# Optimization experiments

Measured on AMD Instinct MI355X. Metric: run time of the kernel, lower is better.

The kernel has to match this reference:

```python
import jax, jax.numpy as jnp
import numpy as np
from functools import partial

SEQ, BATCH, HIDDEN = 2048, 4, 2048
FFN = 1408            # swiglu: h_to_4h outputs 2*FFN
N_EXPERTS = 8
TOP_K = 2
EPS = 1e-20


def setup_inputs() -> dict:
    key = jax.random.key(0)
    k0, k1, k2, k3 = jax.random.split(key, 4)
    x = jax.random.normal(k0, (SEQ, BATCH, HIDDEN), dtype=jnp.float32)
    wg = jax.random.normal(k1, (N_EXPERTS, HIDDEN), dtype=jnp.float32) * 0.02
    w1 = jax.random.normal(k2, (N_EXPERTS, HIDDEN, 2 * FFN), dtype=jnp.float32) * 0.02
    w2 = jax.random.normal(k3, (N_EXPERTS, FFN, HIDDEN), dtype=jnp.float32) * 0.02
    return {"x": x, "wg": wg, "w1": w1, "w2": w2}


def reference(x, wg, w1, w2):
    # x: [S, B, H] (Megatron layout); transpose(0,1) as in MoELayer.forward
    S, B, H = x.shape
    T = B * S
    xt = jnp.transpose(x, (1, 0, 2)).reshape(T, H)  # [T, H]

    # --- TopKGate (greedy, softmax scoring, norm_topk_prob=True) ---
    logits = xt @ wg.T                       # [T, E]
    scores = jax.nn.softmax(logits, axis=-1)
    topk_w, topk_i = jax.lax.top_k(scores, TOP_K)          # [T, K]
    topk_w = topk_w / (jnp.sum(topk_w, axis=-1, keepdims=True) + EPS)

    # combine weights per (token, expert): C[t, e] = sum_k w_k * [idx_k == e]
    C = jnp.zeros((T, N_EXPERTS), dtype=xt.dtype)
    C = C.at[jnp.arange(T)[:, None], topk_i].add(topk_w)   # [T, E]

    # --- Experts: per-expert swiglu MLP, accumulate weighted combine ---
    def step(acc, inputs):
        w1e, w2e, ce = inputs                # [H,2F], [F,H], [T]
        h = xt @ w1e                         # [T, 2F]
        a, b = jnp.split(h, 2, axis=-1)
        y = (jax.nn.silu(a) * b) @ w2e       # [T, H]
        return acc + ce[:, None] * y, None

    out0 = jnp.zeros((T, H), dtype=xt.dtype)
    out, _ = jax.lax.scan(step, out0, (w1, w2, C.T))

    # back to [S, B, H]
    return jnp.transpose(out.reshape(B, S, H), (1, 0, 2))
```

## Files before the change

### kernel.cpp

```cpp
#include <hip/hip_runtime.h>
#include <hip/hip_bf16.h>
#include <cstdint>
#include <cstddef>


#define S_ 2048
#define B_ 4
#define H_ 2048
#define F_ 1408
#define F2_ 2816
#define E_ 8
#define T_ 8192

typedef float f32x4 __attribute__((ext_vector_type(4)));
typedef short s16x8 __attribute__((ext_vector_type(8)));

__device__ __forceinline__ unsigned short f2b(float f) {
  union { unsigned int i; float f; } v; v.f = f;
  unsigned int r = v.i + 0x7FFFu + ((v.i >> 16) & 1u);
  return (unsigned short)(r >> 16);
}
__device__ __forceinline__ unsigned int pkbf(float lo, float hi) {
  __hip_bfloat162 h2 = __float22bfloat162_rn(make_float2(lo, hi));
  union { __hip_bfloat162 v; unsigned int u; } c; c.v = h2; return c.u;
}
__device__ __forceinline__ void gld16(const unsigned short* gp, unsigned short* lp) {
  __builtin_amdgcn_global_load_lds(
      (const __attribute__((address_space(1))) unsigned int*)gp,
      (__attribute__((address_space(3))) unsigned int*)lp, 16, 0, 0);
}


__global__ void zero_kernel(int* ws_i) {
  if (threadIdx.x < 16) ws_i[threadIdx.x] = 0;
}

__global__ __launch_bounds__(256) void cvt_kernel(
    const float* __restrict__ src, unsigned short* __restrict__ dst, int n8) {
  int i = blockIdx.x * 256 + threadIdx.x;
  if (i >= n8) return;
  f32x4 a = *(const f32x4*)(src + (size_t)i * 8);
  f32x4 b = *(const f32x4*)(src + (size_t)i * 8 + 4);
  uint4 u;
  u.x = pkbf(a[0], a[1]); u.y = pkbf(a[2], a[3]);
  u.z = pkbf(b[0], b[1]); u.w = pkbf(b[2], b[3]);
  *(uint4*)(dst + (size_t)i * 8) = u;
}

__global__ __launch_bounds__(256) void tcvt_kernel(
    const float* __restrict__ src, unsigned short* __restrict__ dst,
    int rows, int cols) {
  int e = blockIdx.z;
  int c0 = blockIdx.x * 64, r0 = blockIdx.y * 64;
  const float* s = src + (size_t)e * rows * cols;
  unsigned short* d = dst + (size_t)e * rows * cols;
  __shared__ unsigned short Lt[64][72];
  int tid = threadIdx.x;
  int cl = tid & 63, w = tid >> 6;
#pragma unroll
  for (int i = 0; i < 16; i++) {
    int r = w * 16 + i;
    Lt[cl][r] = f2b(s[(size_t)(r0 + r) * cols + c0 + cl]);
  }
  __syncthreads();
  int cc = tid >> 3, hc = tid & 7;
#pragma unroll
  for (int j = 0; j < 2; j++) {
    int c = cc + j * 32;
    *(uint4*)&d[(size_t)(c0 + c) * rows + r0 + hc * 8] = *(uint4*)&Lt[c][hc * 8];
  }
}

__global__ __launch_bounds__(256) void gate_kernel(
    const float* __restrict__ x, const float* __restrict__ wg,
    int* __restrict__ counts, int* __restrict__ eidx, float* __restrict__ ewt) {
  int wave = threadIdx.x >> 6, lane = threadIdx.x & 63;
  int t = blockIdx.x * 4 + wave;
  int b = t >> 11, s = t & (S_ - 1);
  const float* xrow = x + (size_t)(s * B_ + b) * H_;
  float acc[E_];
#pragma unroll
  for (int e = 0; e < E_; e++) acc[e] = 0.f;
  for (int h0 = lane * 4; h0 < H_; h0 += 256) {
    f32x4 xa = *(const f32x4*)(xrow + h0);
#pragma unroll
    for (int e = 0; e < E_; e++) {
      f32x4 wa = *(const f32x4*)(wg + e * H_ + h0);
      acc[e] += xa[0] * wa[0] + xa[1] * wa[1] + xa[2] * wa[2] + xa[3] * wa[3];
    }
  }
#pragma unroll
  for (int e = 0; e < E_; e++)
    for (int off = 32; off; off >>= 1) acc[e] += __shfl_xor(acc[e], off, 64);
  if (lane == 0) {
    float m = acc[0];
#pragma unroll
    for (int e = 1; e < E_; e++) m = fmaxf(m, acc[e]);
    float ex[E_], ssum = 0.f;
#pragma unroll
    for (int e = 0; e < E_; e++) { ex[e] = __expf(acc[e] - m); ssum += ex[e]; }
    float sc[E_];
#pragma unroll
    for (int e = 0; e < E_; e++) sc[e] = ex[e] / ssum;
    int i1 = 0;
#pragma unroll
    for (int e = 1; e < E_; e++) if (sc[e] > sc[i1]) i1 = e;
    int i2 = (i1 == 0) ? 1 : 0;
#pragma unroll
    for (int e = 0; e < E_; e++) if (e != i1 && sc[e] > sc[i2]) i2 = e;
    float wsum = sc[i1] + sc[i2] + 1e-20f;
    eidx[2 * t] = i1;     ewt[2 * t] = sc[i1] / wsum;
    eidx[2 * t + 1] = i2; ewt[2 * t + 1] = sc[i2] / wsum;
    atomicAdd(&counts[i1], 1);
    atomicAdd(&counts[i2], 1);
  }
}

__global__ void scan_kernel(const int* __restrict__ counts, int* __restrict__ offs) {
  if (threadIdx.x == 0) {
    int run = 0;
    for (int e = 0; e < E_; e++) { offs[e] = run; run += counts[e]; }
  }
}

__global__ void assign_kernel(const int* __restrict__ eidx, const float* __restrict__ ewt,
                              const int* __restrict__ offs, int* __restrict__ cursor,
                              int* __restrict__ rowlist, float* __restrict__ rowwt) {
  int t = blockIdx.x * 256 + threadIdx.x;
  if (t >= T_) return;
#pragma unroll
  for (int k = 0; k < 2; k++) {
    int e = eidx[2 * t + k];
    int pos = atomicAdd(&cursor[e], 1);
    int slot = offs[e] + pos;
    rowlist[slot] = t;
    rowwt[slot] = ewt[2 * t + k];
  }
}

__global__ __launch_bounds__(256) void gemm1_kernel(
    const unsigned short* __restrict__ xb, const unsigned short* __restrict__ w1t,
    const int* __restrict__ counts, const int* __restrict__ offs,
    const int* __restrict__ rowlist, unsigned short* __restrict__ g) {
  int e = blockIdx.z, ft = blockIdx.y, rt = blockIdx.x;
  int ne = counts[e];
  if (rt * 128 >= ne) return;
  int base = offs[e];

  __shared__ unsigned short aL[128 * 32];
  __shared__ unsigned short bLa[64 * 32];
  __shared__ unsigned short bLb[64 * 32];

  int tid = threadIdx.x;
  int lane = tid & 63, wave = tid >> 6;
  int wm = (wave & 1) * 64, wn = (wave >> 1) * 32;
  int quad = lane >> 4, l15 = lane & 15;

  int srow = tid >> 2, kc = tid & 3;
  int t0 = rowlist[base + min(rt * 128 + srow, ne - 1)];
  int t1 = rowlist[base + min(rt * 128 + 64 + srow, ne - 1)];
  const unsigned short* ap0 = xb + (size_t)((t0 & (S_ - 1)) * B_ + (t0 >> 11)) * H_ + kc * 8;
  const unsigned short* ap1 = xb + (size_t)((t1 & (S_ - 1)) * B_ + (t1 >> 11)) * H_ + kc * 8;
  const unsigned short* bpa = w1t + ((size_t)e * F2_ + ft * 64 + srow) * H_ + kc * 8;
  const unsigned short* bpb = bpa + (size_t)F_ * H_;

  unsigned short* aD0 = aL + wave * 512;
  unsigned short* aD1 = aL + 2048 + wave * 512;
  unsigned short* bDa = bLa + wave * 512;
  unsigned short* bDb = bLb + wave * 512;

  f32x4 acc[2][4][2];
#pragma unroll
  for (int h2 = 0; h2 < 2; h2++)
    for (int i = 0; i < 4; i++)
      for (int j = 0; j < 2; j++) acc[h2][i][j] = (f32x4){0.f, 0.f, 0.f, 0.f};

  for (int k0 = 0; k0 < H_; k0 += 32) {
    __syncthreads();
    gld16(ap0 + k0, aD0);
    gld16(ap1 + k0, aD1);
    gld16(bpa + k0, bDa);
    gld16(bpb + k0, bDb);
    __syncthreads();

    s16x8 af[4];
#pragma unroll
    for (int mi = 0; mi < 4; mi++)
      af[mi] = *(const s16x8*)&aL[(wm + mi * 16 + l15) * 32 + quad * 8];
    s16x8 bfa[2], bfb[2];
#pragma unroll
    for (int ni = 0; ni < 2; ni++) {
      bfa[ni] = *(const s16x8*)&bLa[(wn + ni * 16 + l15) * 32 + quad * 8];
      bfb[ni] = *(const s16x8*)&bLb[(wn + ni * 16 + l15) * 32 + quad * 8];
    }
#pragma unroll
    for (int mi = 0; mi < 4; mi++)
#pragma unroll
      for (int ni = 0; ni < 2; ni++) {
        acc[0][mi][ni] = __builtin_amdgcn_mfma_f32_16x16x32_bf16(af[mi], bfa[ni], acc[0][mi][ni], 0, 0, 0);
        acc[1][mi][ni] = __builtin_amdgcn_mfma_f32_16x16x32_bf16(af[mi], bfb[ni], acc[1][mi][ni], 0, 0, 0);
      }
  }

#pragma unroll
  for (int mi = 0; mi < 4; mi++)
#pragma unroll
    for (int ni = 0; ni < 2; ni++)
#pragma unroll
      for (int v = 0; v < 4; v++) {
        int row = wm + mi * 16 + quad * 4 + v;
        if (rt * 128 + row < ne) {
          int col = wn + ni * 16 + l15;
          float a = acc[0][mi][ni][v], bb = acc[1][mi][ni][v];
          float sg = a / (1.f + __expf(-a));
          g[(size_t)(base + rt * 128 + row) * F_ + ft * 64 + col] = f2b(sg * bb);
        }
      }
}

__global__ __launch_bounds__(256) void gemm2_kernel(
    const unsigned short* __restrict__ g, const unsigned short* __restrict__ w2t,
    const int* __restrict__ counts, const int* __restrict__ offs,
    const int* __restrict__ rowlist, const float* __restrict__ rowwt,
    float* __restrict__ out) {
  int e = blockIdx.z, nt = blockIdx.y, rt = blockIdx.x;
  int ne = counts[e];
  if (rt * 128 >= ne) return;
  int base = offs[e];

  __shared__ unsigned short aL[128 * 32];
  __shared__ unsigned short bL[128 * 32];
  __shared__ float rwL[128];
  __shared__ int   toL[128];

  int tid = threadIdx.x;
  int lane = tid & 63, wave = tid >> 6;
  int wm = (wave & 1) * 64, wn = (wave >> 1) * 64;
  int quad = lane >> 4, l15 = lane & 15;

  int srow = tid >> 2, kc = tid & 3;
  int r0c = min(rt * 128 + srow, ne - 1);
  int r1c = min(rt * 128 + 64 + srow, ne - 1);
  const unsigned short* ap0 = g + (size_t)(base + r0c) * F_ + kc * 8;
  const unsigned short* ap1 = g + (size_t)(base + r1c) * F_ + kc * 8;
  const unsigned short* bp0 = w2t + ((size_t)e * H_ + nt * 128 + srow) * F_ + kc * 8;
  const unsigned short* bp1 = bp0 + (size_t)64 * F_;

  unsigned short* aD0 = aL + wave * 512;
  unsigned short* aD1 = aL + 2048 + wave * 512;
  unsigned short* bD0 = bL + wave * 512;
  unsigned short* bD1 = bL + 2048 + wave * 512;

  if (tid < 128) {
    int rr = min(rt * 128 + tid, ne - 1);
    rwL[tid] = rowwt[base + rr];
    int tk = rowlist[base + rr];
    toL[tid] = ((tk & (S_ - 1)) * B_ + (tk >> 11)) * H_;
  }

  f32x4 acc[4][4];
#pragma unroll
  for (int i = 0; i < 4; i++)
    for (int j = 0; j < 4; j++) acc[i][j] = (f32x4){0.f, 0.f, 0.f, 0.f};

  for (int k0 = 0; k0 < F_; k0 += 32) {
    __syncthreads();
    gld16(ap0 + k0, aD0);
    gld16(ap1 + k0, aD1);
    gld16(bp0 + k0, bD0);
    gld16(bp1 + k0, bD1);
    __syncthreads();

    s16x8 af[4];
#pragma unroll
    for (int mi = 0; mi < 4; mi++)
      af[mi] = *(const s16x8*)&aL[(wm + mi * 16 + l15) * 32 + quad * 8];
    s16x8 bf[4];
#pragma unroll
    for (int ni = 0; ni < 4; ni++)
      bf[ni] = *(const s16x8*)&bL[(wn + ni * 16 + l15) * 32 + quad * 8];
#pragma unroll
    for (int mi = 0; mi < 4; mi++)
#pragma unroll
      for (int ni = 0; ni < 4; ni++)
        acc[mi][ni] = __builtin_amdgcn_mfma_f32_16x16x32_bf16(af[mi], bf[ni], acc[mi][ni], 0, 0, 0);
  }

#pragma unroll
  for (int mi = 0; mi < 4; mi++)
#pragma unroll
    for (int ni = 0; ni < 4; ni++)
#pragma unroll
      for (int v = 0; v < 4; v++) {
        int row = wm + mi * 16 + quad * 4 + v;
        if (rt * 128 + row < ne) {
          int col = wn + ni * 16 + l15;
          atomicAdd(&out[(size_t)toL[row] + nt * 128 + col], acc[mi][ni][v] * rwL[row]);
        }
      }
}

extern "C" void kernel_launch(void* const* d_in, const int* in_sizes, int n_in,
                              void* d_out, int out_size, void* d_ws, size_t ws_size,
                              hipStream_t stream) {
  const float* x  = (const float*)d_in[0];
  const float* wg = (const float*)d_in[1];
  const float* w1 = (const float*)d_in[2];
  const float* w2 = (const float*)d_in[3];
  float* out = (float*)d_out;

  char* ws = (char*)d_ws;
  int*   counts  = (int*)(ws + 0);
  int*   cursor  = (int*)(ws + 32);
  int*   offs    = (int*)(ws + 64);
  int*   eidx    = (int*)(ws + 128);
  float* ewt     = (float*)(ws + 65664);
  int*   rowlist = (int*)(ws + 131200);
  float* rowwt   = (float*)(ws + 196736);
  unsigned short* g   = (unsigned short*)(ws + 262272);
  unsigned short* xb  = (unsigned short*)(ws + 46399616);
  unsigned short* w1t = (unsigned short*)(ws + 79954048);
  unsigned short* w2t = (unsigned short*)(ws + 172228736);

  hipMemsetAsync(d_out, 0, (size_t)out_size * sizeof(float), stream);
  zero_kernel<<<1, 64, 0, stream>>>((int*)ws);
  cvt_kernel<<<T_ * H_ / 8 / 256, 256, 0, stream>>>(x, xb, T_ * H_ / 8);
  tcvt_kernel<<<dim3(F2_ / 64, H_ / 64, E_), 256, 0, stream>>>(w1, w1t, H_, F2_);
  tcvt_kernel<<<dim3(H_ / 64, F_ / 64, E_), 256, 0, stream>>>(w2, w2t, F_, H_);
  gate_kernel<<<T_ / 4, 256, 0, stream>>>(x, wg, counts, eidx, ewt);
  scan_kernel<<<1, 64, 0, stream>>>(counts, offs);
  assign_kernel<<<T_ / 256, 256, 0, stream>>>(eidx, ewt, offs, cursor, rowlist, rowwt);
  gemm1_kernel<<<dim3(64, 22, E_), 256, 0, stream>>>(xb, w1t, counts, offs, rowlist, g);
  gemm2_kernel<<<dim3(64, 16, E_), 256, 0, stream>>>(g, w2t, counts, offs, rowlist, rowwt, out);
}
```

Baseline: 1.430 ms.

## Double-buffer LDS tiles in both expert GEMMs with manual vmcnt waits

Both grouped GEMM kernels get two LDS buffers per operand. The global-to-LDS loads for the next-but-one K tile are issued right after the current tile's fragments are read into registers, and explicit s_waitcnt/s_barrier calls replace the two __syncthreads per iteration. This is meant to hide global load latency behind the MFMA work. It doubles LDS use per block, which may lower occupancy, and the correctness of the hand-written vmcnt counts depends on each thread issuing exactly four loads per stage.

```diff
diff --git a/kernel.cpp b/kernel.cpp
--- a/kernel.cpp
+++ b/kernel.cpp
@@ -14,6 +14,12 @@
 
 typedef float f32x4 __attribute__((ext_vector_type(4)));
 typedef short s16x8 __attribute__((ext_vector_type(8)));
+
+#define WAITV4 asm volatile("s_waitcnt vmcnt(4)" ::: "memory")
+#define WAITV0 asm volatile("s_waitcnt vmcnt(0)" ::: "memory")
+#define LGKM0  asm volatile("s_waitcnt lgkmcnt(0)" ::: "memory")
+#define SB()   __builtin_amdgcn_s_barrier()
+#define SCB()  __builtin_amdgcn_sched_barrier(0)
 
 __device__ __forceinline__ unsigned short f2b(float f) {
   union { unsigned int i; float f; } v; v.f = f;
@@ -147,9 +153,9 @@
   if (rt * 128 >= ne) return;
   int base = offs[e];
 
-  __shared__ unsigned short aL[128 * 32];
-  __shared__ unsigned short bLa[64 * 32];
-  __shared__ unsigned short bLb[64 * 32];
+  __shared__ unsigned short aL[2][128 * 32];
+  __shared__ unsigned short bLa[2][64 * 32];
+  __shared__ unsigned short bLb[2][64 * 32];
 
   int tid = threadIdx.x;
   int lane = tid & 63, wave = tid >> 6;
@@ -164,43 +170,51 @@
   const unsigned short* bpa = w1t + ((size_t)e * F2_ + ft * 64 + srow) * H_ + kc * 8;
   const unsigned short* bpb = bpa + (size_t)F_ * H_;
 
-  unsigned short* aD0 = aL + wave * 512;
-  unsigned short* aD1 = aL + 2048 + wave * 512;
-  unsigned short* bDa = bLa + wave * 512;
-  unsigned short* bDb = bLb + wave * 512;
-
   f32x4 acc[2][4][2];
 #pragma unroll
   for (int h2 = 0; h2 < 2; h2++)
     for (int i = 0; i < 4; i++)
       for (int j = 0; j < 2; j++) acc[h2][i][j] = (f32x4){0.f, 0.f, 0.f, 0.f};
 
-  for (int k0 = 0; k0 < H_; k0 += 32) {
-    __syncthreads();
-    gld16(ap0 + k0, aD0);
-    gld16(ap1 + k0, aD1);
-    gld16(bpa + k0, bDa);
-    gld16(bpb + k0, bDb);
-    __syncthreads();
-
-    s16x8 af[4];
-#pragma unroll
-    for (int mi = 0; mi < 4; mi++)
-      af[mi] = *(const s16x8*)&aL[(wm + mi * 16 + l15) * 32 + quad * 8];
-    s16x8 bfa[2], bfb[2];
-#pragma unroll
-    for (int ni = 0; ni < 2; ni++) {
-      bfa[ni] = *(const s16x8*)&bLa[(wn + ni * 16 + l15) * 32 + quad * 8];
-      bfb[ni] = *(const s16x8*)&bLb[(wn + ni * 16 + l15) * 32 + quad * 8];
-    }
-#pragma unroll
-    for (int mi = 0; mi < 4; mi++)
-#pragma unroll
-      for (int ni = 0; ni < 2; ni++) {
-        acc[0][mi][ni] = __builtin_amdgcn_mfma_f32_16x16x32_bf16(af[mi], bfa[ni], acc[0][mi][ni], 0, 0, 0);
-        acc[1][mi][ni] = __builtin_amdgcn_mfma_f32_16x16x32_bf16(af[mi], bfb[ni], acc[1][mi][ni], 0, 0, 0);
-      }
-  }
+#define G1STAGE(buf, kk) do {                                  \
+    gld16(ap0 + (kk), &aL[buf][wave * 512]);                   \
+    gld16(ap1 + (kk), &aL[buf][2048 + wave * 512]);            \
+    gld16(bpa + (kk), &bLa[buf][wave * 512]);                  \
+    gld16(bpb + (kk), &bLb[buf][wave * 512]); } while (0)
+
+#define G1COMP(buf) do {                                                         \
+    s16x8 af[4], vfa[2], vfb[2];                                                 \
+    _Pragma("unroll")                                                            \
+    for (int mi = 0; mi < 4; mi++)                                               \
+      af[mi] = *(const s16x8*)&aL[buf][(wm + mi * 16 + l15) * 32 + quad * 8];    \
+    _Pragma("unroll")                                                            \
+    for (int ni = 0; ni < 2; ni++) {                                             \
+      vfa[ni] = *(const s16x8*)&bLa[buf][(wn + ni * 16 + l15) * 32 + quad * 8];  \
+      vfb[ni] = *(const s16x8*)&bLb[buf][(wn + ni * 16 + l15) * 32 + quad * 8];  \
+    }                                                                            \
+    LGKM0; SB(); SCB();                                                          \
+    if (!lastp) { G1STAGE(buf, knext); }                                         \
+    _Pragma("unroll")                                                            \
+    for (int mi = 0; mi < 4; mi++)                                               \
+      _Pragma("unroll")                                                          \
+      for (int ni = 0; ni < 2; ni++) {                                           \
+        acc[0][mi][ni] = __builtin_amdgcn_mfma_f32_16x16x32_bf16(af[mi], vfa[ni], acc[0][mi][ni], 0, 0, 0); \
+        acc[1][mi][ni] = __builtin_amdgcn_mfma_f32_16x16x32_bf16(af[mi], vfb[ni], acc[1][mi][ni], 0, 0, 0); \
+      } } while (0)
+
+  G1STAGE(0, 0);
+  G1STAGE(1, 32);
+
+  for (int k0 = 0; k0 < H_; k0 += 64) {
+    int lastp = (k0 + 64 >= H_);
+    WAITV4; SB(); SCB();
+    { int knext = k0 + 64; G1COMP(0); }
+    if (lastp) { WAITV0; } else { WAITV4; }
+    SB(); SCB();
+    { int knext = k0 + 96; G1COMP(1); }
+  }
+#undef G1STAGE
+#undef G1COMP
 
 #pragma unroll
   for (int mi = 0; mi < 4; mi++)
@@ -228,8 +242,8 @@
   if (rt * 128 >= ne) return;
   int base = offs[e];
 
-  __shared__ unsigned short aL[128 * 32];
-  __shared__ unsigned short bL[128 * 32];
+  __shared__ unsigned short aL[2][128 * 32];
+  __shared__ unsigned short bL[2][128 * 32];
   __shared__ float rwL[128];
   __shared__ int   toL[128];
 
@@ -246,11 +260,6 @@
   const unsigned short* bp0 = w2t + ((size_t)e * H_ + nt * 128 + srow) * F_ + kc * 8;
   const unsigned short* bp1 = bp0 + (size_t)64 * F_;
 
-  unsigned short* aD0 = aL + wave * 512;
-  unsigned short* aD1 = aL + 2048 + wave * 512;
-  unsigned short* bD0 = bL + wave * 512;
-  unsigned short* bD1 = bL + 2048 + wave * 512;
-
   if (tid < 128) {
     int rr = min(rt * 128 + tid, ne - 1);
     rwL[tid] = rowwt[base + rr];
@@ -263,28 +272,42 @@
   for (int i = 0; i < 4; i++)
     for (int j = 0; j < 4; j++) acc[i][j] = (f32x4){0.f, 0.f, 0.f, 0.f};
 
-  for (int k0 = 0; k0 < F_; k0 += 32) {
-    __syncthreads();
-    gld16(ap0 + k0, aD0);
-    gld16(ap1 + k0, aD1);
-    gld16(bp0 + k0, bD0);
-    gld16(bp1 + k0, bD1);
-    __syncthreads();
-
-    s16x8 af[4];
-#pragma unroll
-    for (int mi = 0; mi < 4; mi++)
-      af[mi] = *(const s16x8*)&aL[(wm + mi * 16 + l15) * 32 + quad * 8];
-    s16x8 bf[4];
-#pragma unroll
-    for (int ni = 0; ni < 4; ni++)
-      bf[ni] = *(const s16x8*)&bL[(wn + ni * 16 + l15) * 32 + quad * 8];
-#pragma unroll
-    for (int mi = 0; mi < 4; mi++)
-#pragma unroll
-      for (int ni = 0; ni < 4; ni++)
-        acc[mi][ni] = __builtin_amdgcn_mfma_f32_16x16x32_bf16(af[mi], bf[ni], acc[mi][ni], 0, 0, 0);
-  }
+#define G2STAGE(buf, kk) do {                                  \
+    gld16(ap0 + (kk), &aL[buf][wave * 512]);                   \
+    gld16(ap1 + (kk), &aL[buf][2048 + wave * 512]);            \
+    gld16(bp0 + (kk), &bL[buf][wave * 512]);                   \
+    gld16(bp1 + (kk), &bL[buf][2048 + wave * 512]); } while (0)
+
+#define G2COMP(buf) do {                                                        \
+    s16x8 af[4], bf[4];                                                         \
+    _Pragma("unroll")                                                           \
+    for (int mi = 0; mi < 4; mi++)                                              \
+      af[mi] = *(const s16x8*)&aL[buf][(wm + mi * 16 + l15) * 32 + quad * 8];   \
+    _Pragma("unroll")                                                           \
+    for (int ni = 0; ni < 4; ni++)                                              \
+      bf[ni] = *(const s16x8*)&bL[buf][(wn + ni * 16 + l15) * 32 + quad * 8];   \
+    LGKM0; SB(); SCB();                                                         \
+    if (!lastp) { G2STAGE(buf, knext); }                                        \
+    _Pragma("unroll")                                                           \
+    for (int mi = 0; mi < 4; mi++)                                              \
+      _Pragma("unroll")                                                         \
+      for (int ni = 0; ni < 4; ni++)                                            \
+        acc[mi][ni] = __builtin_amdgcn_mfma_f32_16x16x32_bf16(af[mi], bf[ni], acc[mi][ni], 0, 0, 0); \
+    } while (0)
+
+  G2STAGE(0, 0);
+  G2STAGE(1, 32);
+
+  for (int k0 = 0; k0 < F_; k0 += 64) {
+    int lastp = (k0 + 64 >= F_);
+    WAITV4; SB(); SCB();
+    { int knext = k0 + 64; G2COMP(0); }
+    if (lastp) { WAITV0; } else { WAITV4; }
+    SB(); SCB();
+    { int knext = k0 + 96; G2COMP(1); }
+  }
+#undef G2STAGE
+#undef G2COMP
 
 #pragma unroll
   for (int mi = 0; mi < 4; mi++)
```

New measurement: 1.377 ms. -3.7%, faster.

## Enlarge expert GEMM tiles and double-buffer swizzled LDS loads

Applied to the files above, without the earlier changes.

Both expert GEMMs move from 128-row tiles with a K step of 32 and 256 threads to 256x256 tiles with a K step of 64 and 512 threads. Global-to-LDS loads are double-buffered and issued two stages ahead, gated by explicit vmcnt waits and barriers. An XOR swizzle on the LDS layout avoids bank conflicts, and s_setprio wraps the MFMA bursts. The aim is more data reuse per byte loaded and overlap of memory traffic with matrix math. The cost is 128KB of LDS per block and heavy register use, which limits occupancy, plus more wasted work on partially filled row tiles when an expert has few tokens.

```diff
diff --git a/kernel.cpp b/kernel.cpp
--- a/kernel.cpp
+++ b/kernel.cpp
@@ -15,6 +15,12 @@
 typedef float f32x4 __attribute__((ext_vector_type(4)));
 typedef short s16x8 __attribute__((ext_vector_type(8)));
 
+#define WAITV8 asm volatile("s_waitcnt vmcnt(8)" ::: "memory")
+#define WAITV0 asm volatile("s_waitcnt vmcnt(0)" ::: "memory")
+#define LGKM0  asm volatile("s_waitcnt lgkmcnt(0)" ::: "memory")
+#define SB()   __builtin_amdgcn_s_barrier()
+#define SCB()  __builtin_amdgcn_sched_barrier(0)
+
 __device__ __forceinline__ unsigned short f2b(float f) {
   union { unsigned int i; float f; } v; v.f = f;
   unsigned int r = v.i + 0x7FFFu + ((v.i >> 16) & 1u);
@@ -28,6 +34,9 @@
   __builtin_amdgcn_global_load_lds(
       (const __attribute__((address_space(1))) unsigned int*)gp,
       (__attribute__((address_space(3))) unsigned int*)lp, 16, 0, 0);
+}
+__device__ __forceinline__ s16x8 ldfrag(const unsigned short* base, int r, int c) {
+  return *(const s16x8*)((const char*)base + r * 128 + (((c) ^ (r & 7)) << 4));
 }
 
 
@@ -138,164 +147,270 @@
   }
 }
 
-__global__ __launch_bounds__(256) void gemm1_kernel(
+__global__ __launch_bounds__(512, 2) void gemm1_kernel(
     const unsigned short* __restrict__ xb, const unsigned short* __restrict__ w1t,
     const int* __restrict__ counts, const int* __restrict__ offs,
     const int* __restrict__ rowlist, unsigned short* __restrict__ g) {
-  int e = blockIdx.z, ft = blockIdx.y, rt = blockIdx.x;
+  int e = blockIdx.z, ft = blockIdx.y, mt = blockIdx.x;
   int ne = counts[e];
-  if (rt * 128 >= ne) return;
+  if (mt * 256 >= ne) return;
   int base = offs[e];
 
-  __shared__ unsigned short aL[128 * 32];
-  __shared__ unsigned short bLa[64 * 32];
-  __shared__ unsigned short bLb[64 * 32];
+  __shared__ unsigned short A_[2][256 * 64];
+  __shared__ unsigned short Bt_[2][256 * 64];
 
   int tid = threadIdx.x;
-  int lane = tid & 63, wave = tid >> 6;
-  int wm = (wave & 1) * 64, wn = (wave >> 1) * 32;
-  int quad = lane >> 4, l15 = lane & 15;
-
-  int srow = tid >> 2, kc = tid & 3;
-  int t0 = rowlist[base + min(rt * 128 + srow, ne - 1)];
-  int t1 = rowlist[base + min(rt * 128 + 64 + srow, ne - 1)];
-  const unsigned short* ap0 = xb + (size_t)((t0 & (S_ - 1)) * B_ + (t0 >> 11)) * H_ + kc * 8;
-  const unsigned short* ap1 = xb + (size_t)((t1 & (S_ - 1)) * B_ + (t1 >> 11)) * H_ + kc * 8;
-  const unsigned short* bpa = w1t + ((size_t)e * F2_ + ft * 64 + srow) * H_ + kc * 8;
-  const unsigned short* bpb = bpa + (size_t)F_ * H_;
-
-  unsigned short* aD0 = aL + wave * 512;
-  unsigned short* aD1 = aL + 2048 + wave * 512;
-  unsigned short* bDa = bLa + wave * 512;
-  unsigned short* bDb = bLb + wave * 512;
-
-  f32x4 acc[2][4][2];
-#pragma unroll
-  for (int h2 = 0; h2 < 2; h2++)
-    for (int i = 0; i < 4; i++)
-      for (int j = 0; j < 2; j++) acc[h2][i][j] = (f32x4){0.f, 0.f, 0.f, 0.f};
-
-  for (int k0 = 0; k0 < H_; k0 += 32) {
-    __syncthreads();
-    gld16(ap0 + k0, aD0);
-    gld16(ap1 + k0, aD1);
-    gld16(bpa + k0, bDa);
-    gld16(bpb + k0, bDb);
-    __syncthreads();
-
-    s16x8 af[4];
-#pragma unroll
-    for (int mi = 0; mi < 4; mi++)
-      af[mi] = *(const s16x8*)&aL[(wm + mi * 16 + l15) * 32 + quad * 8];
-    s16x8 bfa[2], bfb[2];
-#pragma unroll
-    for (int ni = 0; ni < 2; ni++) {
-      bfa[ni] = *(const s16x8*)&bLa[(wn + ni * 16 + l15) * 32 + quad * 8];
-      bfb[ni] = *(const s16x8*)&bLb[(wn + ni * 16 + l15) * 32 + quad * 8];
+  int l = tid & 63, w = tid >> 6;
+  int quad = l >> 4, l15 = l & 15;
+  int wmr = (w & 1) * 128;
+  int wn1 = (w >> 1) * 32;
+
+  int r8 = l >> 3, cg = (l & 7) ^ r8;
+  const unsigned short* apt[4];
+  const unsigned short* bpt[4];
+#pragma unroll
+  for (int j = 0; j < 4; j++) {
+    int R = j * 64 + w * 8 + r8;
+    int tok = rowlist[base + min(mt * 256 + R, ne - 1)];
+    apt[j] = xb + (size_t)((tok & (S_ - 1)) * B_ + (tok >> 11)) * H_ + cg * 8;
+    int brow = (R < 128) ? (ft * 128 + R) : (F_ + ft * 128 + (R - 128));
+    bpt[j] = w1t + ((size_t)e * F2_ + brow) * H_ + cg * 8;
+  }
+
+  f32x4 aa[8][2], ab[8][2];
+#pragma unroll
+  for (int i = 0; i < 8; i++)
+#pragma unroll
+    for (int n = 0; n < 2; n++) {
+      aa[i][n] = (f32x4){0.f, 0.f, 0.f, 0.f};
+      ab[i][n] = (f32x4){0.f, 0.f, 0.f, 0.f};
     }
-#pragma unroll
-    for (int mi = 0; mi < 4; mi++)
-#pragma unroll
-      for (int ni = 0; ni < 2; ni++) {
-        acc[0][mi][ni] = __builtin_amdgcn_mfma_f32_16x16x32_bf16(af[mi], bfa[ni], acc[0][mi][ni], 0, 0, 0);
-        acc[1][mi][ni] = __builtin_amdgcn_mfma_f32_16x16x32_bf16(af[mi], bfb[ni], acc[1][mi][ni], 0, 0, 0);
-      }
-  }
-
-#pragma unroll
-  for (int mi = 0; mi < 4; mi++)
-#pragma unroll
-    for (int ni = 0; ni < 2; ni++)
+
+#define STG1(bf, kk) do {                                         \
+    _Pragma("unroll")                                             \
+    for (int j = 0; j < 4; j++) {                                 \
+      gld16(apt[j] + (kk), &A_[bf][(j * 64 + w * 8) * 64]);       \
+      gld16(bpt[j] + (kk), &Bt_[bf][(j * 64 + w * 8) * 64]);      \
+    } } while (0)
+
+  STG1(0, 0);
+  STG1(1, 64);
+
+  const int NS = H_ / 64;
+  for (int t = 0; t < NS; ++t) {
+    int buf = t & 1;
+    if (t < NS - 1) { WAITV8; } else { WAITV0; }
+    SB(); SCB();
+    const unsigned short* Ab = &A_[buf][0];
+    const unsigned short* Bb = &Bt_[buf][0];
+
+    s16x8 b0a[2], b0b[2];
+#pragma unroll
+    for (int n = 0; n < 2; n++) {
+      b0a[n] = ldfrag(Bb, wn1 + n * 16 + l15, quad);
+      b0b[n] = ldfrag(Bb, 128 + wn1 + n * 16 + l15, quad);
+    }
+    s16x8 af0[4];
+#pragma unroll
+    for (int i = 0; i < 4; i++) af0[i] = ldfrag(Ab, wmr + i * 16 + l15, quad);
+    __builtin_amdgcn_s_setprio(1);
+#pragma unroll
+    for (int i = 0; i < 4; i++)
+#pragma unroll
+      for (int n = 0; n < 2; n++) {
+        aa[i][n] = __builtin_amdgcn_mfma_f32_16x16x32_bf16(af0[i], b0a[n], aa[i][n], 0, 0, 0);
+        ab[i][n] = __builtin_amdgcn_mfma_f32_16x16x32_bf16(af0[i], b0b[n], ab[i][n], 0, 0, 0);
+      }
+    __builtin_amdgcn_s_setprio(0);
+    s16x8 af1[4];
+#pragma unroll
+    for (int i = 0; i < 4; i++) af1[i] = ldfrag(Ab, wmr + (4 + i) * 16 + l15, quad);
+    __builtin_amdgcn_s_setprio(1);
+#pragma unroll
+    for (int i = 0; i < 4; i++)
+#pragma unroll
+      for (int n = 0; n < 2; n++) {
+        aa[4 + i][n] = __builtin_amdgcn_mfma_f32_16x16x32_bf16(af1[i], b0a[n], aa[4 + i][n], 0, 0, 0);
+        ab[4 + i][n] = __builtin_amdgcn_mfma_f32_16x16x32_bf16(af1[i], b0b[n], ab[4 + i][n], 0, 0, 0);
+      }
+    __builtin_amdgcn_s_setprio(0);
+
+    s16x8 b1a[2], b1b[2];
+#pragma unroll
+    for (int n = 0; n < 2; n++) {
+      b1a[n] = ldfrag(Bb, wn1 + n * 16 + l15, 4 + quad);
+      b1b[n] = ldfrag(Bb, 128 + wn1 + n * 16 + l15, 4 + quad);
+    }
+    s16x8 af2[4];
+#pragma unroll
+    for (int i = 0; i < 4; i++) af2[i] = ldfrag(Ab, wmr + i * 16 + l15, 4 + quad);
+    __builtin_amdgcn_s_setprio(1);
+#pragma unroll
+    for (int i = 0; i < 4; i++)
+#pragma unroll
+      for (int n = 0; n < 2; n++) {
+        aa[i][n] = __builtin_amdgcn_mfma_f32_16x16x32_bf16(af2[i], b1a[n], aa[i][n], 0, 0, 0);
+        ab[i][n] = __builtin_amdgcn_mfma_f32_16x16x32_bf16(af2[i], b1b[n], ab[i][n], 0, 0, 0);
+      }
+    __builtin_amdgcn_s_setprio(0);
+    s16x8 af3[4];
+#pragma unroll
+    for (int i = 0; i < 4; i++) af3[i] = ldfrag(Ab, wmr + (4 + i) * 16 + l15, 4 + quad);
+    LGKM0; SB(); SCB();
+    if (t + 2 < NS) STG1(buf, (t + 2) * 64);
+    __builtin_amdgcn_s_setprio(1);
+#pragma unroll
+    for (int i = 0; i < 4; i++)
+#pragma unroll
+      for (int n = 0; n < 2; n++) {
+        aa[4 + i][n] = __builtin_amdgcn_mfma_f32_16x16x32_bf16(af3[i], b1a[n], aa[4 + i][n], 0, 0, 0);
+        ab[4 + i][n] = __builtin_amdgcn_mfma_f32_16x16x32_bf16(af3[i], b1b[n], ab[4 + i][n], 0, 0, 0);
+      }
+    __builtin_amdgcn_s_setprio(0);
+  }
+#undef STG1
+
+#pragma unroll
+  for (int i = 0; i < 8; i++)
+#pragma unroll
+    for (int n = 0; n < 2; n++)
 #pragma unroll
       for (int v = 0; v < 4; v++) {
-        int row = wm + mi * 16 + quad * 4 + v;
-        if (rt * 128 + row < ne) {
-          int col = wn + ni * 16 + l15;
-          float a = acc[0][mi][ni][v], bb = acc[1][mi][ni][v];
+        int row = wmr + i * 16 + quad * 4 + v;
+        if (mt * 256 + row < ne) {
+          int col = ft * 128 + wn1 + n * 16 + l15;
+          float a = aa[i][n][v], bb = ab[i][n][v];
           float sg = a / (1.f + __expf(-a));
-          g[(size_t)(base + rt * 128 + row) * F_ + ft * 64 + col] = f2b(sg * bb);
+          g[(size_t)(base + mt * 256 + row) * F_ + col] = f2b(sg * bb);
         }
       }
 }
 
-__global__ __launch_bounds__(256) void gemm2_kernel(
+__global__ __launch_bounds__(512, 2) void gemm2_kernel(
     const unsigned short* __restrict__ g, const unsigned short* __restrict__ w2t,
     const int* __restrict__ counts, const int* __restrict__ offs,
     const int* __restrict__ rowlist, const float* __restrict__ rowwt,
     float* __restrict__ out) {
-  int e = blockIdx.z, nt = blockIdx.y, rt = blockIdx.x;
+  int e = blockIdx.z, nt = blockIdx.y, mt = blockIdx.x;
   int ne = counts[e];
-  if (rt * 128 >= ne) return;
+  if (mt * 256 >= ne) return;
   int base = offs[e];
 
-  __shared__ unsigned short aL[128 * 32];
-  __shared__ unsigned short bL[128 * 32];
-  __shared__ float rwL[128];
-  __shared__ int   toL[128];
+  __shared__ unsigned short A_[2][256 * 64];
+  __shared__ unsigned short Bt_[2][256 * 64];
+  __shared__ float rwL[256];
+  __shared__ int   toL[256];
 
   int tid = threadIdx.x;
-  int lane = tid & 63, wave = tid >> 6;
-  int wm = (wave & 1) * 64, wn = (wave >> 1) * 64;
-  int quad = lane >> 4, l15 = lane & 15;
-
-  int srow = tid >> 2, kc = tid & 3;
-  int r0c = min(rt * 128 + srow, ne - 1);
-  int r1c = min(rt * 128 + 64 + srow, ne - 1);
-  const unsigned short* ap0 = g + (size_t)(base + r0c) * F_ + kc * 8;
-  const unsigned short* ap1 = g + (size_t)(base + r1c) * F_ + kc * 8;
-  const unsigned short* bp0 = w2t + ((size_t)e * H_ + nt * 128 + srow) * F_ + kc * 8;
-  const unsigned short* bp1 = bp0 + (size_t)64 * F_;
-
-  unsigned short* aD0 = aL + wave * 512;
-  unsigned short* aD1 = aL + 2048 + wave * 512;
-  unsigned short* bD0 = bL + wave * 512;
-  unsigned short* bD1 = bL + 2048 + wave * 512;
-
-  if (tid < 128) {
-    int rr = min(rt * 128 + tid, ne - 1);
+  int l = tid & 63, w = tid >> 6;
+  int quad = l >> 4, l15 = l & 15;
+  int wmr = (w & 1) * 128;
+  int wn2 = (w >> 1) * 64;
+
+  int r8 = l >> 3, cg = (l & 7) ^ r8;
+  const unsigned short* apt[4];
+  const unsigned short* bpt[4];
+#pragma unroll
+  for (int j = 0; j < 4; j++) {
+    int R = j * 64 + w * 8 + r8;
+    int arow = min(mt * 256 + R, ne - 1);
+    apt[j] = g + (size_t)(base + arow) * F_ + cg * 8;
+    bpt[j] = w2t + ((size_t)e * H_ + nt * 256 + R) * F_ + cg * 8;
+  }
+
+  if (tid < 256) {
+    int rr = min(mt * 256 + tid, ne - 1);
     rwL[tid] = rowwt[base + rr];
     int tk = rowlist[base + rr];
     toL[tid] = ((tk & (S_ - 1)) * B_ + (tk >> 11)) * H_;
   }
 
-  f32x4 acc[4][4];
-#pragma unroll
-  for (int i = 0; i < 4; i++)
-    for (int j = 0; j < 4; j++) acc[i][j] = (f32x4){0.f, 0.f, 0.f, 0.f};
-
-  for (int k0 = 0; k0 < F_; k0 += 32) {
-    __syncthreads();
-    gld16(ap0 + k0, aD0);
-    gld16(ap1 + k0, aD1);
-    gld16(bp0 + k0, bD0);
-    gld16(bp1 + k0, bD1);
-    __syncthreads();
-
-    s16x8 af[4];
-#pragma unroll
-    for (int mi = 0; mi < 4; mi++)
-      af[mi] = *(const s16x8*)&aL[(wm + mi * 16 + l15) * 32 + quad * 8];
-    s16x8 bf[4];
-#pragma unroll
-    for (int ni = 0; ni < 4; ni++)
-      bf[ni] = *(const s16x8*)&bL[(wn + ni * 16 + l15) * 32 + quad * 8];
-#pragma unroll
-    for (int mi = 0; mi < 4; mi++)
-#pragma unroll
-      for (int ni = 0; ni < 4; ni++)
-        acc[mi][ni] = __builtin_amdgcn_mfma_f32_16x16x32_bf16(af[mi], bf[ni], acc[mi][ni], 0, 0, 0);
-  }
-
-#pragma unroll
-  for (int mi = 0; mi < 4; mi++)
-#pragma unroll
-    for (int ni = 0; ni < 4; ni++)
+  f32x4 acc[8][4];
+#pragma unroll
+  for (int i = 0; i < 8; i++)
+#pragma unroll
+    for (int n = 0; n < 4; n++) acc[i][n] = (f32x4){0.f, 0.f, 0.f, 0.f};
+
+#define STG2(bf, kk) do {                                         \
+    _Pragma("unroll")                                             \
+    for (int j = 0; j < 4; j++) {                                 \
+      gld16(apt[j] + (kk), &A_[bf][(j * 64 + w * 8) * 64]);       \
+      gld16(bpt[j] + (kk), &Bt_[bf][(j * 64 + w * 8) * 64]);      \
+    } } while (0)
+
+  STG2(0, 0);
+  STG2(1, 64);
+
+  const int NS = F_ / 64;
+  for (int t = 0; t < NS; ++t) {
+    int buf = t & 1;
+    if (t < NS - 1) { WAITV8; } else { WAITV0; }
+    SB(); SCB();
+    const unsigned short* Ab = &A_[buf][0];
+    const unsigned short* Bb = &Bt_[buf][0];
+
+    s16x8 b0[4];
+#pragma unroll
+    for (int n = 0; n < 4; n++) b0[n] = ldfrag(Bb, wn2 + n * 16 + l15, quad);
+    s16x8 af0[4];
+#pragma unroll
+    for (int i = 0; i < 4; i++) af0[i] = ldfrag(Ab, wmr + i * 16 + l15, quad);
+    __builtin_amdgcn_s_setprio(1);
+#pragma unroll
+    for (int i = 0; i < 4; i++)
+#pragma unroll
+      for (int n = 0; n < 4; n++)
+        acc[i][n] = __builtin_amdgcn_mfma_f32_16x16x32_bf16(af0[i], b0[n], acc[i][n], 0, 0, 0);
+    __builtin_amdgcn_s_setprio(0);
+    s16x8 af1[4];
+#pragma unroll
+    for (int i = 0; i < 4; i++) af1[i] = ldfrag(Ab, wmr + (4 + i) * 16 + l15, quad);
+    __builtin_amdgcn_s_setprio(1);
+#pragma unroll
+    for (int i = 0; i < 4; i++)
+#pragma unroll
+      for (int n = 0; n < 4; n++)
+        acc[4 + i][n] = __builtin_amdgcn_mfma_f32_16x16x32_bf16(af1[i], b0[n], acc[4 + i][n], 0, 0, 0);
+    __builtin_amdgcn_s_setprio(0);
+
+    s16x8 b1[4];
+#pragma unroll
+    for (int n = 0; n < 4; n++) b1[n] = ldfrag(Bb, wn2 + n * 16 + l15, 4 + quad);
+    s16x8 af2[4];
+#pragma unroll
+    for (int i = 0; i < 4; i++) af2[i] = ldfrag(Ab, wmr + i * 16 + l15, 4 + quad);
+    __builtin_amdgcn_s_setprio(1);
+#pragma unroll
+    for (int i = 0; i < 4; i++)
+#pragma unroll
+      for (int n = 0; n < 4; n++)
+        acc[i][n] = __builtin_amdgcn_mfma_f32_16x16x32_bf16(af2[i], b1[n], acc[i][n], 0, 0, 0);
+    __builtin_amdgcn_s_setprio(0);
+    s16x8 af3[4];
+#pragma unroll
+    for (int i = 0; i < 4; i++) af3[i] = ldfrag(Ab, wmr + (4 + i) * 16 + l15, 4 + quad);
+    LGKM0; SB(); SCB();
+    if (t + 2 < NS) STG2(buf, (t + 2) * 64);
+    __builtin_amdgcn_s_setprio(1);
+#pragma unroll
+    for (int i = 0; i < 4; i++)
+#pragma unroll
+      for (int n = 0; n < 4; n++)
+        acc[4 + i][n] = __builtin_amdgcn_mfma_f32_16x16x32_bf16(af3[i], b1[n], acc[4 + i][n], 0, 0, 0);
+    __builtin_amdgcn_s_setprio(0);
+  }
+#undef STG2
+
+#pragma unroll
+  for (int i = 0; i < 8; i++)
+#pragma unroll
+    for (int n = 0; n < 4; n++)
 #pragma unroll
       for (int v = 0; v < 4; v++) {
-        int row = wm + mi * 16 + quad * 4 + v;
-        if (rt * 128 + row < ne) {
-          int col = wn + ni * 16 + l15;
-          atomicAdd(&out[(size_t)toL[row] + nt * 128 + col], acc[mi][ni][v] * rwL[row]);
+        int row = wmr + i * 16 + quad * 4 + v;
+        if (mt * 256 + row < ne) {
+          int col = nt * 256 + wn2 + n * 16 + l15;
+          atomicAdd(&out[(size_t)toL[row] + col], acc[i][n][v] * rwL[row]);
         }
       }
 }
@@ -330,6 +445,6 @@
   gate_kernel<<<T_ / 4, 256, 0, stream>>>(x, wg, counts, eidx, ewt);
   scan_kernel<<<1, 64, 0, stream>>>(counts, offs);
   assign_kernel<<<T_ / 256, 256, 0, stream>>>(eidx, ewt, offs, cursor, rowlist, rowwt);
-  gemm1_kernel<<<dim3(64, 22, E_), 256, 0, stream>>>(xb, w1t, counts, offs, rowlist, g);
-  gemm2_kernel<<<dim3(64, 16, E_), 256, 0, stream>>>(g, w2t, counts, offs, rowlist, rowwt, out);
-}
+  gemm1_kernel<<<dim3(32, F_ / 128, E_), 512, 0, stream>>>(xb, w1t, counts, offs, rowlist, g);
+  gemm2_kernel<<<dim3(32, H_ / 256, E_), 512, 0, stream>>>(g, w2t, counts, offs, rowlist, rowwt, out);
+}
```

New measurement: 1.887 ms. 1.32x slower.
